# Performance work log

Hardware: AMD Instinct MI355X
Metric: run time of the kernel (lower is better)

Reference implementation:

```python
import jax, jax.numpy as jnp
import numpy as np

B, L, C, H = 4, 1024, 768, 12
D = C // H  # head_ch = 64


def setup_inputs() -> dict:
    key = jax.random.key(0)
    ks = jax.random.split(key, 8)
    s = 1.0 / np.sqrt(C)
    return {
        "inputs_q": jax.random.normal(ks[0], (B, L, C), jnp.float32),
        "inputs_kv": jax.random.normal(ks[1], (B, L, C), jnp.float32),
        "Wq": jax.random.normal(ks[2], (C, H * D), jnp.float32) * s,
        "Wk": jax.random.normal(ks[3], (C, H * D), jnp.float32) * s,
        "Wv": jax.random.normal(ks[4], (C, H * D), jnp.float32) * s,
        "Wout": jax.random.normal(ks[5], (H * D, C), jnp.float32) * s,
        "W_pre": jax.random.normal(ks[6], (H, H), jnp.float32) * (1.0 / np.sqrt(H)),
        "W_post": jax.random.normal(ks[7], (H, H), jnp.float32) * (1.0 / np.sqrt(H)),
    }


def reference(inputs_q, inputs_kv, Wq, Wk, Wv, Wout, W_pre, W_post):
    # Linear projections (no bias), split into heads: b l (h d) -> b h l d
    def split_heads(x):
        b, l, _ = x.shape
        return x.reshape(b, l, H, D).transpose(0, 2, 1, 3)

    q = split_heads(inputs_q @ Wq) / jnp.sqrt(jnp.asarray(D, inputs_q.dtype))
    k = split_heads(inputs_kv @ Wk)
    v = split_heads(inputs_kv @ Wv)

    # Attention logits [b, h, l, k]
    weights = jnp.einsum('bhld,bhkd->bhlk', q, k)
    # Talking-heads: learned cross-head mixing pre-softmax
    weights = jnp.einsum('bhlk,hi->bilk', weights, W_pre)
    weights = jax.nn.softmax(weights, axis=-1)
    # Talking-heads post-softmax mixing
    weights = jnp.einsum('bhlk,hi->bilk', weights, W_post)

    scores = jnp.einsum('bhlk,bhkd->bhld', weights, v)
    scores = scores.transpose(0, 2, 1, 3).reshape(B, L, H * D)  # b l (h d)
    return scores @ Wout
```

## Files before the change

kernel.cpp:

```cpp
#include <hip/hip_runtime.h>

#define BB 4
#define LL 1024
#define CC 768
#define HH 12
#define DD 64

typedef unsigned short ushort_t;
typedef __attribute__((ext_vector_type(8))) short bf16x8;
typedef __attribute__((ext_vector_type(4))) float f32x4;

__device__ inline ushort_t f2bf(float x) {
    union { float f; unsigned u; } v; v.f = x;
    unsigned r = (v.u + 0x7FFFu + ((v.u >> 16) & 1u)) >> 16;
    return (ushort_t)r;
}
__device__ inline float bf2f(ushort_t u) {
    union { unsigned u; float f; } v; v.u = ((unsigned)u) << 16;
    return v.f;
}

__device__ inline void stage_rows(const ushort_t* __restrict__ g, int stride,
                                  ushort_t* lds, int nbytes, int wave, int lane) {
    const int ko = (lane & 3) << 3;
    const int rsub = lane >> 2;
    for (int off = wave * 1024; off < nbytes; off += 4096) {
        int row = (off >> 6) + rsub;
        __builtin_amdgcn_global_load_lds(
            (const __attribute__((address_space(1))) void*)(g + (size_t)row * stride + ko),
            (__attribute__((address_space(3))) void*)(lds + (off >> 1)),
            16, 0, 0);
    }
}

__global__ __launch_bounds__(256) void cast_in(const float* __restrict__ q,
                                               const float* __restrict__ kv,
                                               ushort_t* __restrict__ qo,
                                               ushort_t* __restrict__ kvo) {
    const float* src = blockIdx.y ? kv : q;
    ushort_t* dst = blockIdx.y ? kvo : qo;
    size_t i = ((size_t)blockIdx.x * 256 + threadIdx.x) * 8;
    float4 a = *(const float4*)(src + i);
    float4 b = *(const float4*)(src + i + 4);
    ushort_t t[8] = {f2bf(a.x), f2bf(a.y), f2bf(a.z), f2bf(a.w),
                     f2bf(b.x), f2bf(b.y), f2bf(b.z), f2bf(b.w)};
    *(uint4*)(dst + i) = *(uint4*)t;
}

__global__ __launch_bounds__(256) void wt_cast(const float* __restrict__ w0, const float* __restrict__ w1,
                                               const float* __restrict__ w2, const float* __restrict__ w3,
                                               ushort_t* __restrict__ o0, ushort_t* __restrict__ o1,
                                               ushort_t* __restrict__ o2, ushort_t* __restrict__ o3) {
    const float* W = blockIdx.z == 0 ? w0 : blockIdx.z == 1 ? w1 : blockIdx.z == 2 ? w2 : w3;
    ushort_t* Wt   = blockIdx.z == 0 ? o0 : blockIdx.z == 1 ? o1 : blockIdx.z == 2 ? o2 : o3;
    __shared__ float t[32][33];
    const int c = threadIdx.x & 31, r0 = threadIdx.x >> 5;
    const int kb = blockIdx.x * 32, nb = blockIdx.y * 32;
#pragma unroll
    for (int i = 0; i < 4; ++i)
        t[r0 + 8 * i][c] = W[(size_t)(kb + r0 + 8 * i) * CC + nb + c];
    __syncthreads();
#pragma unroll
    for (int i = 0; i < 4; ++i)
        Wt[(size_t)(nb + r0 + 8 * i) * CC + kb + c] = f2bf(t[c][r0 + 8 * i]);
}

__global__ __launch_bounds__(256) void proj_gemm(const ushort_t* __restrict__ Aq,
                                                 const ushort_t* __restrict__ Akv,
                                                 const ushort_t* __restrict__ Wqt,
                                                 const ushort_t* __restrict__ Wkt,
                                                 const ushort_t* __restrict__ Wvt,
                                                 ushort_t* __restrict__ Qo,
                                                 ushort_t* __restrict__ Ko,
                                                 ushort_t* __restrict__ Vto) {
    const int z = blockIdx.z;
    const ushort_t* A  = (z == 0) ? Aq : Akv;
    const ushort_t* Wt = (z == 0) ? Wqt : (z == 1 ? Wkt : Wvt);

    __shared__ __align__(16) ushort_t a_lds[128 * 32];
    __shared__ __align__(16) ushort_t b_lds[128 * 32];

    const int tid = threadIdx.x;
    const int bm = blockIdx.x * 128, bn = blockIdx.y * 128;
    const int wave = tid >> 6, lane = tid & 63;
    const int quad = lane >> 4, lq = lane & 15;
    const int wr = wave >> 1, wc = wave & 1;

    f32x4 acc[4][4] = {};

    for (int k0 = 0; k0 < CC; k0 += 32) {
        stage_rows(A + (size_t)bm * CC + k0, CC, a_lds, 8192, wave, lane);
        stage_rows(Wt + (size_t)bn * CC + k0, CC, b_lds, 8192, wave, lane);
        __syncthreads();
        bf16x8 af[4], bfr[4];
#pragma unroll
        for (int mi = 0; mi < 4; ++mi)
            af[mi] = *(bf16x8*)&a_lds[(wr * 64 + mi * 16 + lq) * 32 + quad * 8];
#pragma unroll
        for (int ni = 0; ni < 4; ++ni)
            bfr[ni] = *(bf16x8*)&b_lds[(wc * 64 + ni * 16 + lq) * 32 + quad * 8];
#pragma unroll
        for (int mi = 0; mi < 4; ++mi)
#pragma unroll
            for (int ni = 0; ni < 4; ++ni)
                acc[mi][ni] = __builtin_amdgcn_mfma_f32_16x16x32_bf16(af[mi], bfr[ni], acc[mi][ni], 0, 0, 0);
        __syncthreads();
    }

    const float scale = (z == 0) ? 0.125f : 1.0f;
#pragma unroll
    for (int mi = 0; mi < 4; ++mi)
#pragma unroll
        for (int ni = 0; ni < 4; ++ni)
#pragma unroll
            for (int r = 0; r < 4; ++r) {
                int row = bm + wr * 64 + mi * 16 + quad * 4 + r;
                int col = bn + wc * 64 + ni * 16 + lq;
                int b = row >> 10, l = row & 1023, h = col >> 6, d = col & 63;
                ushort_t v = f2bf(acc[mi][ni][r] * scale);
                if (z == 0)      Qo[((size_t)(b * HH + h) * LL + l) * DD + d] = v;
                else if (z == 1) Ko[((size_t)(b * HH + h) * LL + l) * DD + d] = v;
                else             Vto[((size_t)(b * HH + h) * DD + d) * LL + l] = v;
            }
}

__global__ __launch_bounds__(256) void qk_gemm(const ushort_t* __restrict__ Q,
                                               const ushort_t* __restrict__ K,
                                               ushort_t* __restrict__ S) {
    __shared__ __align__(16) ushort_t a_lds[128 * 32];
    __shared__ __align__(16) ushort_t b_lds[128 * 32];

    const int tid = threadIdx.x;
    const int bm = blockIdx.x * 128, bn = blockIdx.y * 128;
    const int bh = blockIdx.z;
    const ushort_t* Qh = Q + (size_t)bh * LL * DD;
    const ushort_t* Kh = K + (size_t)bh * LL * DD;
    const int wave = tid >> 6, lane = tid & 63;
    const int quad = lane >> 4, lq = lane & 15;
    const int wr = wave >> 1, wc = wave & 1;

    f32x4 acc[4][4] = {};

    for (int k0 = 0; k0 < DD; k0 += 32) {
        stage_rows(Qh + (size_t)bm * DD + k0, DD, a_lds, 8192, wave, lane);
        stage_rows(Kh + (size_t)bn * DD + k0, DD, b_lds, 8192, wave, lane);
        __syncthreads();
        bf16x8 af[4], bfr[4];
#pragma unroll
        for (int mi = 0; mi < 4; ++mi)
            af[mi] = *(bf16x8*)&a_lds[(wr * 64 + mi * 16 + lq) * 32 + quad * 8];
#pragma unroll
        for (int ni = 0; ni < 4; ++ni)
            bfr[ni] = *(bf16x8*)&b_lds[(wc * 64 + ni * 16 + lq) * 32 + quad * 8];
#pragma unroll
        for (int mi = 0; mi < 4; ++mi)
#pragma unroll
            for (int ni = 0; ni < 4; ++ni)
                acc[mi][ni] = __builtin_amdgcn_mfma_f32_16x16x32_bf16(af[mi], bfr[ni], acc[mi][ni], 0, 0, 0);
        __syncthreads();
    }

#pragma unroll
    for (int mi = 0; mi < 4; ++mi)
#pragma unroll
        for (int ni = 0; ni < 4; ++ni)
#pragma unroll
            for (int r = 0; r < 4; ++r) {
                int row = bm + wr * 64 + mi * 16 + quad * 4 + r;
                int col = bn + wc * 64 + ni * 16 + lq;
                S[((size_t)bh * LL + row) * LL + col] = f2bf(acc[mi][ni][r]);
            }
}

__global__ __launch_bounds__(256) void mix_softmax(ushort_t* __restrict__ S,
                                                   const float* __restrict__ Wpre,
                                                   const float* __restrict__ Wpost) {
    __shared__ float s[HH][LL];
    __shared__ float wpre[HH][HH];
    __shared__ float wpost[HH][HH];

    const int tid = threadIdx.x;
    const int l = blockIdx.x;
    const int b = blockIdx.y;

    if (tid < HH * HH) {
        wpre[tid / HH][tid % HH] = Wpre[tid];
        wpost[tid / HH][tid % HH] = Wpost[tid];
    }

    for (int idx = tid; idx < HH * 256; idx += 256) {
        int h = idx >> 8, c = idx & 255;
        uint2 raw = *(const uint2*)&S[((size_t)(b * HH + h) * LL + l) * LL + c * 4];
        ushort_t* u = (ushort_t*)&raw;
        float4 f = make_float4(bf2f(u[0]), bf2f(u[1]), bf2f(u[2]), bf2f(u[3]));
        ((float4*)s[h])[c] = f;
    }
    __syncthreads();

    for (int k = tid; k < LL; k += 256) {
        float sv[HH], mx[HH];
#pragma unroll
        for (int h = 0; h < HH; ++h) sv[h] = s[h][k];
#pragma unroll
        for (int i = 0; i < HH; ++i) {
            float a = 0.f;
#pragma unroll
            for (int h = 0; h < HH; ++h) a += sv[h] * wpre[h][i];
            mx[i] = a;
        }
#pragma unroll
        for (int i = 0; i < HH; ++i) s[i][k] = mx[i];
    }
    __syncthreads();

    {
        const int wave = tid >> 6;
        const int lane = tid & 63;
        for (int h = wave; h < HH; h += 4) {
            float vals[16];
            float m = -1e30f;
#pragma unroll
            for (int j = 0; j < 16; ++j) {
                vals[j] = s[h][lane + 64 * j];
                m = fmaxf(m, vals[j]);
            }
#pragma unroll
            for (int off = 32; off; off >>= 1) m = fmaxf(m, __shfl_xor(m, off));
            float sum = 0.f;
#pragma unroll
            for (int j = 0; j < 16; ++j) {
                vals[j] = __expf(vals[j] - m);
                sum += vals[j];
            }
#pragma unroll
            for (int off = 32; off; off >>= 1) sum += __shfl_xor(sum, off);
            float inv = 1.0f / sum;
#pragma unroll
            for (int j = 0; j < 16; ++j) s[h][lane + 64 * j] = vals[j] * inv;
        }
    }
    __syncthreads();

    for (int k = tid; k < LL; k += 256) {
        float sv[HH], mx[HH];
#pragma unroll
        for (int h = 0; h < HH; ++h) sv[h] = s[h][k];
#pragma unroll
        for (int i = 0; i < HH; ++i) {
            float a = 0.f;
#pragma unroll
            for (int h = 0; h < HH; ++h) a += sv[h] * wpost[h][i];
            mx[i] = a;
        }
#pragma unroll
        for (int i = 0; i < HH; ++i) s[i][k] = mx[i];
    }
    __syncthreads();

    for (int idx = tid; idx < HH * 256; idx += 256) {
        int h = idx >> 8, c = idx & 255;
        float4 f = ((float4*)s[h])[c];
        ushort_t u[4] = {f2bf(f.x), f2bf(f.y), f2bf(f.z), f2bf(f.w)};
        *(uint2*)&S[((size_t)(b * HH + h) * LL + l) * LL + c * 4] = *(uint2*)u;
    }
}

__global__ __launch_bounds__(256) void pv_gemm(const ushort_t* __restrict__ P,
                                               const ushort_t* __restrict__ Vt,
                                               ushort_t* __restrict__ att) {
    __shared__ __align__(16) ushort_t a_lds[64 * 32];
    __shared__ __align__(16) ushort_t b_lds[64 * 32];

    const int tid = threadIdx.x;
    const int bm = blockIdx.x * 64;
    const int bh = blockIdx.y;
    const int b = bh / HH, ih = bh % HH;
    const ushort_t* Ph = P + ((size_t)bh << 20);
    const ushort_t* Vh = Vt + (size_t)bh * LL * DD;
    const int wave = tid >> 6, lane = tid & 63;
    const int quad = lane >> 4, lq = lane & 15;
    const int wr = wave >> 1, wc = wave & 1;

    f32x4 acc[2][2] = {};

    for (int k0 = 0; k0 < LL; k0 += 32) {
        stage_rows(Ph + (size_t)bm * LL + k0, LL, a_lds, 4096, wave, lane);
        stage_rows(Vh + k0, LL, b_lds, 4096, wave, lane);
        __syncthreads();
        bf16x8 af[2], bfr[2];
#pragma unroll
        for (int mi = 0; mi < 2; ++mi)
            af[mi] = *(bf16x8*)&a_lds[(wr * 32 + mi * 16 + lq) * 32 + quad * 8];
#pragma unroll
        for (int ni = 0; ni < 2; ++ni)
            bfr[ni] = *(bf16x8*)&b_lds[(wc * 32 + ni * 16 + lq) * 32 + quad * 8];
#pragma unroll
        for (int mi = 0; mi < 2; ++mi)
#pragma unroll
            for (int ni = 0; ni < 2; ++ni)
                acc[mi][ni] = __builtin_amdgcn_mfma_f32_16x16x32_bf16(af[mi], bfr[ni], acc[mi][ni], 0, 0, 0);
        __syncthreads();
    }

#pragma unroll
    for (int mi = 0; mi < 2; ++mi)
#pragma unroll
        for (int ni = 0; ni < 2; ++ni)
#pragma unroll
            for (int r = 0; r < 4; ++r) {
                int lrow = bm + wr * 32 + mi * 16 + quad * 4 + r;
                int col = wc * 32 + ni * 16 + lq;
                att[((size_t)(b * LL) + lrow) * CC + ih * DD + col] = f2bf(acc[mi][ni][r]);
            }
}

__global__ __launch_bounds__(256) void out_gemm(const ushort_t* __restrict__ A,
                                                const ushort_t* __restrict__ Wt,
                                                float* __restrict__ out) {
    __shared__ __align__(16) ushort_t a_lds[128 * 32];
    __shared__ __align__(16) ushort_t b_lds[128 * 32];

    const int tid = threadIdx.x;
    const int bm = blockIdx.x * 128, bn = blockIdx.y * 128;
    const int wave = tid >> 6, lane = tid & 63;
    const int quad = lane >> 4, lq = lane & 15;
    const int wr = wave >> 1, wc = wave & 1;

    f32x4 acc[4][4] = {};

    for (int k0 = 0; k0 < CC; k0 += 32) {
        stage_rows(A + (size_t)bm * CC + k0, CC, a_lds, 8192, wave, lane);
        stage_rows(Wt + (size_t)bn * CC + k0, CC, b_lds, 8192, wave, lane);
        __syncthreads();
        bf16x8 af[4], bfr[4];
#pragma unroll
        for (int mi = 0; mi < 4; ++mi)
            af[mi] = *(bf16x8*)&a_lds[(wr * 64 + mi * 16 + lq) * 32 + quad * 8];
#pragma unroll
        for (int ni = 0; ni < 4; ++ni)
            bfr[ni] = *(bf16x8*)&b_lds[(wc * 64 + ni * 16 + lq) * 32 + quad * 8];
#pragma unroll
        for (int mi = 0; mi < 4; ++mi)
#pragma unroll
            for (int ni = 0; ni < 4; ++ni)
                acc[mi][ni] = __builtin_amdgcn_mfma_f32_16x16x32_bf16(af[mi], bfr[ni], acc[mi][ni], 0, 0, 0);
        __syncthreads();
    }

#pragma unroll
    for (int mi = 0; mi < 4; ++mi)
#pragma unroll
        for (int ni = 0; ni < 4; ++ni)
#pragma unroll
            for (int r = 0; r < 4; ++r) {
                int row = bm + wr * 64 + mi * 16 + quad * 4 + r;
                int col = bn + wc * 64 + ni * 16 + lq;
                out[(size_t)row * CC + col] = acc[mi][ni][r];
            }
}

extern "C" void kernel_launch(void* const* d_in, const int* in_sizes, int n_in,
                              void* d_out, int out_size, void* d_ws, size_t ws_size,
                              hipStream_t stream) {
    const float* inputs_q  = (const float*)d_in[0];
    const float* inputs_kv = (const float*)d_in[1];
    const float* Wq   = (const float*)d_in[2];
    const float* Wk   = (const float*)d_in[3];
    const float* Wv   = (const float*)d_in[4];
    const float* Wout = (const float*)d_in[5];
    const float* Wpre  = (const float*)d_in[6];
    const float* Wpost = (const float*)d_in[7];
    float* out = (float*)d_out;

    const size_t nS   = (size_t)BB * HH * LL * LL;
    const size_t nQKV = (size_t)BB * HH * LL * DD;
    const size_t nW   = (size_t)CC * CC;

    ushort_t* Sb   = (ushort_t*)d_ws;
    ushort_t* Qb   = Sb + nS;
    ushort_t* Kb   = Qb + nQKV;
    ushort_t* Vtb  = Kb + nQKV;
    ushort_t* attb = Vtb + nQKV;
    ushort_t* inq  = attb + nQKV;
    ushort_t* inkv = inq + nQKV;
    ushort_t* Wqt  = inkv + nQKV;
    ushort_t* Wkt  = Wqt + nW;
    ushort_t* Wvt  = Wkt + nW;
    ushort_t* Wot  = Wvt + nW;

    dim3 blk(256);

    cast_in<<<dim3(1536, 2), blk, 0, stream>>>(inputs_q, inputs_kv, inq, inkv);
    wt_cast<<<dim3(24, 24, 4), blk, 0, stream>>>(Wq, Wk, Wv, Wout, Wqt, Wkt, Wvt, Wot);
    proj_gemm<<<dim3(32, 6, 3), blk, 0, stream>>>(inq, inkv, Wqt, Wkt, Wvt, Qb, Kb, Vtb);
    qk_gemm<<<dim3(8, 8, BB * HH), blk, 0, stream>>>(Qb, Kb, Sb);
    mix_softmax<<<dim3(LL, BB), blk, 0, stream>>>(Sb, Wpre, Wpost);
    pv_gemm<<<dim3(16, BB * HH), blk, 0, stream>>>(Sb, Vtb, attb);
    out_gemm<<<dim3(32, 6), blk, 0, stream>>>(attb, Wot, out);
}
```

Measured before the change: 272.4 us.

## Fuse prep casts, register-resident mix_softmax, and narrower out_gemm tiles

Merges the input cast and weight transpose-cast kernels into one launch. It also rewrites mix_softmax so each thread keeps its 4 columns for all 12 heads in registers. That removes the 48KB LDS staging buffer and most barriers, which should raise occupancy of this memory-bound pass. The out_gemm tile shrinks from 128x128 to 128x64, doubling the block count to 384 so more CUs are filled, at the cost of more A-tile reloads.

```diff
diff --git a/kernel.cpp b/kernel.cpp
--- a/kernel.cpp
+++ b/kernel.cpp
@@ -33,36 +33,39 @@
     }
 }
 
-__global__ __launch_bounds__(256) void cast_in(const float* __restrict__ q,
-                                               const float* __restrict__ kv,
-                                               ushort_t* __restrict__ qo,
-                                               ushort_t* __restrict__ kvo) {
-    const float* src = blockIdx.y ? kv : q;
-    ushort_t* dst = blockIdx.y ? kvo : qo;
-    size_t i = ((size_t)blockIdx.x * 256 + threadIdx.x) * 8;
-    float4 a = *(const float4*)(src + i);
-    float4 b = *(const float4*)(src + i + 4);
-    ushort_t t[8] = {f2bf(a.x), f2bf(a.y), f2bf(a.z), f2bf(a.w),
-                     f2bf(b.x), f2bf(b.y), f2bf(b.z), f2bf(b.w)};
-    *(uint4*)(dst + i) = *(uint4*)t;
-}
-
-__global__ __launch_bounds__(256) void wt_cast(const float* __restrict__ w0, const float* __restrict__ w1,
-                                               const float* __restrict__ w2, const float* __restrict__ w3,
-                                               ushort_t* __restrict__ o0, ushort_t* __restrict__ o1,
-                                               ushort_t* __restrict__ o2, ushort_t* __restrict__ o3) {
-    const float* W = blockIdx.z == 0 ? w0 : blockIdx.z == 1 ? w1 : blockIdx.z == 2 ? w2 : w3;
-    ushort_t* Wt   = blockIdx.z == 0 ? o0 : blockIdx.z == 1 ? o1 : blockIdx.z == 2 ? o2 : o3;
+__global__ __launch_bounds__(256) void prep(const float* __restrict__ q, const float* __restrict__ kv,
+                                            const float* __restrict__ w0, const float* __restrict__ w1,
+                                            const float* __restrict__ w2, const float* __restrict__ w3,
+                                            ushort_t* __restrict__ qo, ushort_t* __restrict__ kvo,
+                                            ushort_t* __restrict__ o0, ushort_t* __restrict__ o1,
+                                            ushort_t* __restrict__ o2, ushort_t* __restrict__ o3) {
     __shared__ float t[32][33];
-    const int c = threadIdx.x & 31, r0 = threadIdx.x >> 5;
-    const int kb = blockIdx.x * 32, nb = blockIdx.y * 32;
-#pragma unroll
-    for (int i = 0; i < 4; ++i)
-        t[r0 + 8 * i][c] = W[(size_t)(kb + r0 + 8 * i) * CC + nb + c];
-    __syncthreads();
-#pragma unroll
-    for (int i = 0; i < 4; ++i)
-        Wt[(size_t)(nb + r0 + 8 * i) * CC + kb + c] = f2bf(t[c][r0 + 8 * i]);
+    const int bx = blockIdx.x;
+    if (bx < 3072) {
+        const float* src = bx < 1536 ? q : kv;
+        ushort_t* dst = bx < 1536 ? qo : kvo;
+        int bb = bx < 1536 ? bx : bx - 1536;
+        size_t i = ((size_t)bb * 256 + threadIdx.x) * 8;
+        float4 a = *(const float4*)(src + i);
+        float4 b = *(const float4*)(src + i + 4);
+        ushort_t u[8] = {f2bf(a.x), f2bf(a.y), f2bf(a.z), f2bf(a.w),
+                         f2bf(b.x), f2bf(b.y), f2bf(b.z), f2bf(b.w)};
+        *(uint4*)(dst + i) = *(uint4*)u;
+    } else {
+        int w = bx - 3072;
+        int z = w / 576, rem = w % 576;
+        const float* W = z == 0 ? w0 : z == 1 ? w1 : z == 2 ? w2 : w3;
+        ushort_t* Wt   = z == 0 ? o0 : z == 1 ? o1 : z == 2 ? o2 : o3;
+        const int c = threadIdx.x & 31, r0 = threadIdx.x >> 5;
+        const int kb = (rem / 24) * 32, nb = (rem % 24) * 32;
+#pragma unroll
+        for (int i = 0; i < 4; ++i)
+            t[r0 + 8 * i][c] = W[(size_t)(kb + r0 + 8 * i) * CC + nb + c];
+        __syncthreads();
+#pragma unroll
+        for (int i = 0; i < 4; ++i)
+            Wt[(size_t)(nb + r0 + 8 * i) * CC + kb + c] = f2bf(t[c][r0 + 8 * i]);
+    }
 }
 
 __global__ __launch_bounds__(256) void proj_gemm(const ushort_t* __restrict__ Aq,
@@ -175,93 +178,101 @@
 __global__ __launch_bounds__(256) void mix_softmax(ushort_t* __restrict__ S,
                                                    const float* __restrict__ Wpre,
                                                    const float* __restrict__ Wpost) {
-    __shared__ float s[HH][LL];
-    __shared__ float wpre[HH][HH];
-    __shared__ float wpost[HH][HH];
+    __shared__ float wpre[HH * HH];
+    __shared__ float wpostT[HH * HH];
+    __shared__ float redm[4][16];
+    __shared__ float reds[4][16];
 
     const int tid = threadIdx.x;
-    const int l = blockIdx.x;
-    const int b = blockIdx.y;
+    const int wave = tid >> 6, lane = tid & 63;
+    const int l = blockIdx.x, b = blockIdx.y;
 
     if (tid < HH * HH) {
-        wpre[tid / HH][tid % HH] = Wpre[tid];
-        wpost[tid / HH][tid % HH] = Wpost[tid];
-    }
-
-    for (int idx = tid; idx < HH * 256; idx += 256) {
-        int h = idx >> 8, c = idx & 255;
-        uint2 raw = *(const uint2*)&S[((size_t)(b * HH + h) * LL + l) * LL + c * 4];
-        ushort_t* u = (ushort_t*)&raw;
-        float4 f = make_float4(bf2f(u[0]), bf2f(u[1]), bf2f(u[2]), bf2f(u[3]));
-        ((float4*)s[h])[c] = f;
+        wpre[tid] = Wpre[tid];
+        wpostT[(tid % HH) * HH + tid / HH] = Wpost[tid];
     }
     __syncthreads();
 
-    for (int k = tid; k < LL; k += 256) {
-        float sv[HH], mx[HH];
-#pragma unroll
-        for (int h = 0; h < HH; ++h) sv[h] = s[h][k];
+    const size_t hstride = (size_t)LL * LL;
+    const size_t base = ((size_t)(b * HH) * LL + l) * LL + tid * 4;
+
+    float p[HH][4];
+#pragma unroll
+    for (int i = 0; i < HH; ++i)
+        p[i][0] = p[i][1] = p[i][2] = p[i][3] = 0.f;
+#pragma unroll
+    for (int h = 0; h < HH; ++h) {
+        uint2 raw = *(const uint2*)&S[base + h * hstride];
+        const ushort_t* u = (const ushort_t*)&raw;
+        float v0 = bf2f(u[0]), v1 = bf2f(u[1]), v2 = bf2f(u[2]), v3 = bf2f(u[3]);
+        const float4 w0 = *(const float4*)&wpre[h * HH + 0];
+        const float4 w1 = *(const float4*)&wpre[h * HH + 4];
+        const float4 w2 = *(const float4*)&wpre[h * HH + 8];
+        const float wv[12] = {w0.x, w0.y, w0.z, w0.w, w1.x, w1.y, w1.z, w1.w,
+                              w2.x, w2.y, w2.z, w2.w};
 #pragma unroll
         for (int i = 0; i < HH; ++i) {
-            float a = 0.f;
-#pragma unroll
-            for (int h = 0; h < HH; ++h) a += sv[h] * wpre[h][i];
-            mx[i] = a;
+            p[i][0] += v0 * wv[i]; p[i][1] += v1 * wv[i];
+            p[i][2] += v2 * wv[i]; p[i][3] += v3 * wv[i];
         }
-#pragma unroll
-        for (int i = 0; i < HH; ++i) s[i][k] = mx[i];
+    }
+
+    float m[HH];
+#pragma unroll
+    for (int i = 0; i < HH; ++i) {
+        float mm = fmaxf(fmaxf(p[i][0], p[i][1]), fmaxf(p[i][2], p[i][3]));
+#pragma unroll
+        for (int off = 32; off; off >>= 1) mm = fmaxf(mm, __shfl_xor(mm, off));
+        m[i] = mm;
+    }
+    if (lane == 0) {
+#pragma unroll
+        for (int i = 0; i < HH; ++i) redm[wave][i] = m[i];
     }
     __syncthreads();
-
-    {
-        const int wave = tid >> 6;
-        const int lane = tid & 63;
-        for (int h = wave; h < HH; h += 4) {
-            float vals[16];
-            float m = -1e30f;
-#pragma unroll
-            for (int j = 0; j < 16; ++j) {
-                vals[j] = s[h][lane + 64 * j];
-                m = fmaxf(m, vals[j]);
-            }
-#pragma unroll
-            for (int off = 32; off; off >>= 1) m = fmaxf(m, __shfl_xor(m, off));
-            float sum = 0.f;
-#pragma unroll
-            for (int j = 0; j < 16; ++j) {
-                vals[j] = __expf(vals[j] - m);
-                sum += vals[j];
-            }
-#pragma unroll
-            for (int off = 32; off; off >>= 1) sum += __shfl_xor(sum, off);
-            float inv = 1.0f / sum;
-#pragma unroll
-            for (int j = 0; j < 16; ++j) s[h][lane + 64 * j] = vals[j] * inv;
+#pragma unroll
+    for (int i = 0; i < HH; ++i)
+        m[i] = fmaxf(fmaxf(redm[0][i], redm[1][i]), fmaxf(redm[2][i], redm[3][i]));
+
+    float sm[HH];
+#pragma unroll
+    for (int i = 0; i < HH; ++i) {
+        p[i][0] = __expf(p[i][0] - m[i]);
+        p[i][1] = __expf(p[i][1] - m[i]);
+        p[i][2] = __expf(p[i][2] - m[i]);
+        p[i][3] = __expf(p[i][3] - m[i]);
+        float ss = (p[i][0] + p[i][1]) + (p[i][2] + p[i][3]);
+#pragma unroll
+        for (int off = 32; off; off >>= 1) ss += __shfl_xor(ss, off);
+        sm[i] = ss;
+    }
+    if (lane == 0) {
+#pragma unroll
+        for (int i = 0; i < HH; ++i) reds[wave][i] = sm[i];
+    }
+    __syncthreads();
+#pragma unroll
+    for (int i = 0; i < HH; ++i) {
+        float tot = (reds[0][i] + reds[1][i]) + (reds[2][i] + reds[3][i]);
+        float inv = 1.0f / tot;
+        p[i][0] *= inv; p[i][1] *= inv; p[i][2] *= inv; p[i][3] *= inv;
+    }
+
+#pragma unroll
+    for (int i = 0; i < HH; ++i) {
+        const float4 w0 = *(const float4*)&wpostT[i * HH + 0];
+        const float4 w1 = *(const float4*)&wpostT[i * HH + 4];
+        const float4 w2 = *(const float4*)&wpostT[i * HH + 8];
+        const float wv[12] = {w0.x, w0.y, w0.z, w0.w, w1.x, w1.y, w1.z, w1.w,
+                              w2.x, w2.y, w2.z, w2.w};
+        float a0 = 0.f, a1 = 0.f, a2 = 0.f, a3 = 0.f;
+#pragma unroll
+        for (int h = 0; h < HH; ++h) {
+            a0 += p[h][0] * wv[h]; a1 += p[h][1] * wv[h];
+            a2 += p[h][2] * wv[h]; a3 += p[h][3] * wv[h];
         }
-    }
-    __syncthreads();
-
-    for (int k = tid; k < LL; k += 256) {
-        float sv[HH], mx[HH];
-#pragma unroll
-        for (int h = 0; h < HH; ++h) sv[h] = s[h][k];
-#pragma unroll
-        for (int i = 0; i < HH; ++i) {
-            float a = 0.f;
-#pragma unroll
-            for (int h = 0; h < HH; ++h) a += sv[h] * wpost[h][i];
-            mx[i] = a;
-        }
-#pragma unroll
-        for (int i = 0; i < HH; ++i) s[i][k] = mx[i];
-    }
-    __syncthreads();
-
-    for (int idx = tid; idx < HH * 256; idx += 256) {
-        int h = idx >> 8, c = idx & 255;
-        float4 f = ((float4*)s[h])[c];
-        ushort_t u[4] = {f2bf(f.x), f2bf(f.y), f2bf(f.z), f2bf(f.w)};
-        *(uint2*)&S[((size_t)(b * HH + h) * LL + l) * LL + c * 4] = *(uint2*)u;
+        ushort_t u[4] = {f2bf(a0), f2bf(a1), f2bf(a2), f2bf(a3)};
+        *(uint2*)&S[base + i * hstride] = *(uint2*)u;
     }
 }
 
@@ -318,31 +329,31 @@
                                                 const ushort_t* __restrict__ Wt,
                                                 float* __restrict__ out) {
     __shared__ __align__(16) ushort_t a_lds[128 * 32];
-    __shared__ __align__(16) ushort_t b_lds[128 * 32];
+    __shared__ __align__(16) ushort_t b_lds[64 * 32];
 
     const int tid = threadIdx.x;
-    const int bm = blockIdx.x * 128, bn = blockIdx.y * 128;
+    const int bm = blockIdx.x * 128, bn = blockIdx.y * 64;
     const int wave = tid >> 6, lane = tid & 63;
     const int quad = lane >> 4, lq = lane & 15;
     const int wr = wave >> 1, wc = wave & 1;
 
-    f32x4 acc[4][4] = {};
+    f32x4 acc[4][2] = {};
 
     for (int k0 = 0; k0 < CC; k0 += 32) {
         stage_rows(A + (size_t)bm * CC + k0, CC, a_lds, 8192, wave, lane);
-        stage_rows(Wt + (size_t)bn * CC + k0, CC, b_lds, 8192, wave, lane);
-        __syncthreads();
-        bf16x8 af[4], bfr[4];
+        stage_rows(Wt + (size_t)bn * CC + k0, CC, b_lds, 4096, wave, lane);
+        __syncthreads();
+        bf16x8 af[4], bfr[2];
 #pragma unroll
         for (int mi = 0; mi < 4; ++mi)
             af[mi] = *(bf16x8*)&a_lds[(wr * 64 + mi * 16 + lq) * 32 + quad * 8];
 #pragma unroll
-        for (int ni = 0; ni < 4; ++ni)
-            bfr[ni] = *(bf16x8*)&b_lds[(wc * 64 + ni * 16 + lq) * 32 + quad * 8];
-#pragma unroll
-        for (int mi = 0; mi < 4; ++mi)
-#pragma unroll
-            for (int ni = 0; ni < 4; ++ni)
+        for (int ni = 0; ni < 2; ++ni)
+            bfr[ni] = *(bf16x8*)&b_lds[(wc * 32 + ni * 16 + lq) * 32 + quad * 8];
+#pragma unroll
+        for (int mi = 0; mi < 4; ++mi)
+#pragma unroll
+            for (int ni = 0; ni < 2; ++ni)
                 acc[mi][ni] = __builtin_amdgcn_mfma_f32_16x16x32_bf16(af[mi], bfr[ni], acc[mi][ni], 0, 0, 0);
         __syncthreads();
     }
@@ -350,11 +361,11 @@
 #pragma unroll
     for (int mi = 0; mi < 4; ++mi)
 #pragma unroll
-        for (int ni = 0; ni < 4; ++ni)
+        for (int ni = 0; ni < 2; ++ni)
 #pragma unroll
             for (int r = 0; r < 4; ++r) {
                 int row = bm + wr * 64 + mi * 16 + quad * 4 + r;
-                int col = bn + wc * 64 + ni * 16 + lq;
+                int col = bn + wc * 32 + ni * 16 + lq;
                 out[(size_t)row * CC + col] = acc[mi][ni][r];
             }
 }
@@ -390,11 +401,11 @@
 
     dim3 blk(256);
 
-    cast_in<<<dim3(1536, 2), blk, 0, stream>>>(inputs_q, inputs_kv, inq, inkv);
-    wt_cast<<<dim3(24, 24, 4), blk, 0, stream>>>(Wq, Wk, Wv, Wout, Wqt, Wkt, Wvt, Wot);
+    prep<<<dim3(5376), blk, 0, stream>>>(inputs_q, inputs_kv, Wq, Wk, Wv, Wout,
+                                         inq, inkv, Wqt, Wkt, Wvt, Wot);
     proj_gemm<<<dim3(32, 6, 3), blk, 0, stream>>>(inq, inkv, Wqt, Wkt, Wvt, Qb, Kb, Vtb);
     qk_gemm<<<dim3(8, 8, BB * HH), blk, 0, stream>>>(Qb, Kb, Sb);
     mix_softmax<<<dim3(LL, BB), blk, 0, stream>>>(Sb, Wpre, Wpost);
     pv_gemm<<<dim3(16, BB * HH), blk, 0, stream>>>(Sb, Vtb, attb);
-    out_gemm<<<dim3(32, 6), blk, 0, stream>>>(attb, Wot, out);
-}
+    out_gemm<<<dim3(32, 12), blk, 0, stream>>>(attb, Wot, out);
+}
```

Result: faster. 242.5 us (-11.0%).
